# Optimization experiments

Measured on AMD Instinct MI355X. Metric: run time of the kernel, lower is better.

The kernel has to match this reference:

```python
import jax, jax.numpy as jnp
import numpy as np

B, C, T, R = 32, 8, 512, 256


def setup_inputs() -> dict:
    key = jax.random.key(0)
    k1, k2, k3 = jax.random.split(key, 3)
    x = jax.random.normal(k1, (B, C, T), dtype=jnp.float32)
    # W_in ~ U(-1, 1), shape [reservoir, input_size=1]
    W_in = jax.random.uniform(k2, (R, 1), minval=-1.0, maxval=1.0, dtype=jnp.float32)
    # diagonal of W_res ~ U(-1, 1)
    d = jax.random.uniform(k3, (R,), minval=-1.0, maxval=1.0, dtype=jnp.float32)
    return {"x": x, "W_in": W_in, "d": d}


def reference(x, W_in, d):
    # state_{t} = tanh(u_t * W_in[:,0] + state_{t-1} * d), vectorized over (B,C)
    w = W_in[:, 0]                       # [R]
    b, c, t = x.shape
    xs = jnp.moveaxis(x, -1, 0)          # [T, B, C]
    init = jnp.zeros((b, c, w.shape[0]), dtype=x.dtype)  # [B, C, R]

    def step(state, u_t):
        s = jnp.tanh(u_t[..., None] * w + state * d)  # [B, C, R]
        return s, s

    _, states = jax.lax.scan(step, init, xs)  # [T, B, C, R]
    return jnp.moveaxis(states, 0, 2)         # [B, C, T, R]
```

## Files before the change

### kernel.cpp

```cpp
#include <hip/hip_runtime.h>


constexpr int Bdim = 32;
constexpr int Cdim = 8;
constexpr int Tdim = 512;
constexpr int Rdim = 256;
constexpr int T4   = Tdim / 4;
constexpr int NT   = 128;

__device__ __forceinline__ float fast_exp2(float v) {
#if defined(__has_builtin)
#if __has_builtin(__builtin_amdgcn_exp2f)
    return __builtin_amdgcn_exp2f(v);
#else
    return exp2f(v);
#endif
#else
    return exp2f(v);
#endif
}

__global__ __launch_bounds__(NT, 1) void esn_scan_kernel(
    const float* __restrict__ x,
    const float* __restrict__ W_in,
    const float* __restrict__ d,
    float* __restrict__ out)
{
    const int bc = blockIdx.x;
    const int i  = threadIdx.x;

    const float K     = 2.0f * 1.4426950408889634f;
    const float wkA   = W_in[i] * K;
    const float dkA   = d[i] * K;
    const float m2dkA = -2.0f * dkA;
    const float wkB   = W_in[i + 128] * K;
    const float dkB   = d[i + 128] * K;
    const float m2dkB = -2.0f * dkB;

    __shared__ float4 xs4[T4];
    {
        const float4* __restrict__ x4 = reinterpret_cast<const float4*>(x + bc * Tdim);
        xs4[i] = x4[i];
    }
    __syncthreads();

    float* __restrict__ o = out + (size_t)bc * Tdim * Rdim + i;

    float4 a0 = xs4[0], a1 = xs4[1];
    float4 b0 = xs4[2], b1 = xs4[3];

    float eargA = a0.x * wkA;
    float eargB = a0.x * wkB;

    #pragma unroll 1
    for (int g = 0; g < Tdim / 8; ++g) {
        int pf = 2 * g + 4; if (pf > T4 - 2) pf = T4 - 2;
        float4 c0 = xs4[pf], c1 = xs4[pf + 1];

        float preA[8], preB[8];
        preA[0] = fmaf(a0.y, wkA, dkA);  preB[0] = fmaf(a0.y, wkB, dkB);
        preA[1] = fmaf(a0.z, wkA, dkA);  preB[1] = fmaf(a0.z, wkB, dkB);
        preA[2] = fmaf(a0.w, wkA, dkA);  preB[2] = fmaf(a0.w, wkB, dkB);
        preA[3] = fmaf(a1.x, wkA, dkA);  preB[3] = fmaf(a1.x, wkB, dkB);
        preA[4] = fmaf(a1.y, wkA, dkA);  preB[4] = fmaf(a1.y, wkB, dkB);
        preA[5] = fmaf(a1.z, wkA, dkA);  preB[5] = fmaf(a1.z, wkB, dkB);
        preA[6] = fmaf(a1.w, wkA, dkA);  preB[6] = fmaf(a1.w, wkB, dkB);
        preA[7] = fmaf(b0.x, wkA, dkA);  preB[7] = fmaf(b0.x, wkB, dkB);

        float* ob  = o + (size_t)(g * 8) * Rdim;
        float* ob4 = ob + (size_t)4 * Rdim;

        #pragma unroll
        for (int j = 0; j < 4; ++j) {
            float eA  = fast_exp2(eargA);
            float eB  = fast_exp2(eargB);
            float rcA = __builtin_amdgcn_rcpf(eA + 1.0f);
            float rcB = __builtin_amdgcn_rcpf(eB + 1.0f);
            ob[j * Rdim]       = fmaf(-2.0f, rcA, 1.0f);
            ob[j * Rdim + 128] = fmaf(-2.0f, rcB, 1.0f);
            eargA = fmaf(m2dkA, rcA, preA[j]);
            eargB = fmaf(m2dkB, rcB, preB[j]);
        }
        #pragma unroll
        for (int j = 0; j < 4; ++j) {
            float eA  = fast_exp2(eargA);
            float eB  = fast_exp2(eargB);
            float rcA = __builtin_amdgcn_rcpf(eA + 1.0f);
            float rcB = __builtin_amdgcn_rcpf(eB + 1.0f);
            ob4[j * Rdim]       = fmaf(-2.0f, rcA, 1.0f);
            ob4[j * Rdim + 128] = fmaf(-2.0f, rcB, 1.0f);
            eargA = fmaf(m2dkA, rcA, preA[j + 4]);
            eargB = fmaf(m2dkB, rcB, preB[j + 4]);
        }

        a0 = b0; a1 = b1;
        b0 = c0; b1 = c1;
    }
}

extern "C" void kernel_launch(void* const* d_in, const int* in_sizes, int n_in,
                              void* d_out, int out_size, void* d_ws, size_t ws_size,
                              hipStream_t stream) {
    const float* x    = (const float*)d_in[0];
    const float* W_in = (const float*)d_in[1];
    const float* d    = (const float*)d_in[2];
    float* out        = (float*)d_out;

    dim3 grid(Bdim * Cdim);
    dim3 block(NT);
    esn_scan_kernel<<<grid, block, 0, stream>>>(x, W_in, d, out);
}
```

Baseline: 31.78 us.

## Replace exp2/rcp tanh with clamped rational polynomial and use one thread per reservoir unit

Computes tanh with a clamped rational polynomial approximation (one rcp, no exp) instead of the exp2-plus-reciprocal form. The recurrence now carries the pre-activation directly. The block grows from 128 to 256 threads, so each thread owns one reservoir element instead of two interleaved chains. This shortens the per-step dependency chain by dropping the transcendental, but adds more FMAs per step and slightly changes accuracy near the clamp.

```diff
diff --git a/kernel.cpp b/kernel.cpp
--- a/kernel.cpp
+++ b/kernel.cpp
@@ -6,91 +6,79 @@
 constexpr int Tdim = 512;
 constexpr int Rdim = 256;
 constexpr int T4   = Tdim / 4;
-constexpr int NT   = 128;
 
-__device__ __forceinline__ float fast_exp2(float v) {
-#if defined(__has_builtin)
-#if __has_builtin(__builtin_amdgcn_exp2f)
-    return __builtin_amdgcn_exp2f(v);
-#else
-    return exp2f(v);
-#endif
-#else
-    return exp2f(v);
-#endif
+__device__ __forceinline__ float tanh_p(float z) {
+    float p = fmaf(z, -2.76076847742355e-16f, 2.00018790482477e-13f);
+    p = fmaf(z, p, -8.60467152213735e-11f);
+    p = fmaf(z, p, 5.12229709037114e-08f);
+    p = fmaf(z, p, 1.48572235717979e-05f * 0.0f + 1.48572235717979e-05f);
+    p = fmaf(z, p, 6.37261928875436e-04f);
+    p = fmaf(z, p, 4.89352455891786e-03f);
+    return p;
+}
+__device__ __forceinline__ float tanh_q(float z) {
+    float q = fmaf(z, 1.19825839466702e-06f, 1.18534705686654e-04f);
+    q = fmaf(z, q, 2.26843463243900e-03f);
+    q = fmaf(z, q, 4.89352518554385e-03f);
+    return q;
 }
 
-__global__ __launch_bounds__(NT, 1) void esn_scan_kernel(
+__global__ __launch_bounds__(256, 1) void esn_scan_kernel(
     const float* __restrict__ x,
     const float* __restrict__ W_in,
     const float* __restrict__ d,
     float* __restrict__ out)
 {
     const int bc = blockIdx.x;
-    const int i  = threadIdx.x;
+    const int r  = threadIdx.x;
 
-    const float K     = 2.0f * 1.4426950408889634f;
-    const float wkA   = W_in[i] * K;
-    const float dkA   = d[i] * K;
-    const float m2dkA = -2.0f * dkA;
-    const float wkB   = W_in[i + 128] * K;
-    const float dkB   = d[i + 128] * K;
-    const float m2dkB = -2.0f * dkB;
+    const float wc = W_in[r];
+    const float dc = d[r];
 
     __shared__ float4 xs4[T4];
     {
         const float4* __restrict__ x4 = reinterpret_cast<const float4*>(x + bc * Tdim);
-        xs4[i] = x4[i];
+        if (r < T4) xs4[r] = x4[r];
     }
     __syncthreads();
 
-    float* __restrict__ o = out + (size_t)bc * Tdim * Rdim + i;
+    float* __restrict__ o = out + (size_t)bc * Tdim * Rdim + r;
 
     float4 a0 = xs4[0], a1 = xs4[1];
     float4 b0 = xs4[2], b1 = xs4[3];
 
-    float eargA = a0.x * wkA;
-    float eargB = a0.x * wkB;
+    float a = a0.x * wc;
 
     #pragma unroll 1
     for (int g = 0; g < Tdim / 8; ++g) {
         int pf = 2 * g + 4; if (pf > T4 - 2) pf = T4 - 2;
         float4 c0 = xs4[pf], c1 = xs4[pf + 1];
 
-        float preA[8], preB[8];
-        preA[0] = fmaf(a0.y, wkA, dkA);  preB[0] = fmaf(a0.y, wkB, dkB);
-        preA[1] = fmaf(a0.z, wkA, dkA);  preB[1] = fmaf(a0.z, wkB, dkB);
-        preA[2] = fmaf(a0.w, wkA, dkA);  preB[2] = fmaf(a0.w, wkB, dkB);
-        preA[3] = fmaf(a1.x, wkA, dkA);  preB[3] = fmaf(a1.x, wkB, dkB);
-        preA[4] = fmaf(a1.y, wkA, dkA);  preB[4] = fmaf(a1.y, wkB, dkB);
-        preA[5] = fmaf(a1.z, wkA, dkA);  preB[5] = fmaf(a1.z, wkB, dkB);
-        preA[6] = fmaf(a1.w, wkA, dkA);  preB[6] = fmaf(a1.w, wkB, dkB);
-        preA[7] = fmaf(b0.x, wkA, dkA);  preB[7] = fmaf(b0.x, wkB, dkB);
+        float pre[8];
+        pre[0] = a0.y * wc;
+        pre[1] = a0.z * wc;
+        pre[2] = a0.w * wc;
+        pre[3] = a1.x * wc;
+        pre[4] = a1.y * wc;
+        pre[5] = a1.z * wc;
+        pre[6] = a1.w * wc;
+        pre[7] = b0.x * wc;
 
         float* ob  = o + (size_t)(g * 8) * Rdim;
         float* ob4 = ob + (size_t)4 * Rdim;
 
         #pragma unroll
-        for (int j = 0; j < 4; ++j) {
-            float eA  = fast_exp2(eargA);
-            float eB  = fast_exp2(eargB);
-            float rcA = __builtin_amdgcn_rcpf(eA + 1.0f);
-            float rcB = __builtin_amdgcn_rcpf(eB + 1.0f);
-            ob[j * Rdim]       = fmaf(-2.0f, rcA, 1.0f);
-            ob[j * Rdim + 128] = fmaf(-2.0f, rcB, 1.0f);
-            eargA = fmaf(m2dkA, rcA, preA[j]);
-            eargB = fmaf(m2dkB, rcB, preB[j]);
-        }
-        #pragma unroll
-        for (int j = 0; j < 4; ++j) {
-            float eA  = fast_exp2(eargA);
-            float eB  = fast_exp2(eargB);
-            float rcA = __builtin_amdgcn_rcpf(eA + 1.0f);
-            float rcB = __builtin_amdgcn_rcpf(eB + 1.0f);
-            ob4[j * Rdim]       = fmaf(-2.0f, rcA, 1.0f);
-            ob4[j * Rdim + 128] = fmaf(-2.0f, rcB, 1.0f);
-            eargA = fmaf(m2dkA, rcA, preA[j + 4]);
-            eargB = fmaf(m2dkB, rcB, preB[j + 4]);
+        for (int j = 0; j < 8; ++j) {
+            float z  = a * a;
+            float p  = tanh_p(z);
+            float q  = tanh_q(z);
+            float rc = __builtin_amdgcn_rcpf(q);
+            float pa = p * a;
+            float s  = pa * rc;
+            if (j < 4) ob[j * Rdim] = s;
+            else       ob4[(j - 4) * Rdim] = s;
+            a = fmaf(pa * dc, rc, pre[j]);
+            a = fminf(7.90531f, fmaxf(-7.90531f, a));
         }
 
         a0 = b0; a1 = b1;
@@ -107,6 +95,6 @@
     float* out        = (float*)d_out;
 
     dim3 grid(Bdim * Cdim);
-    dim3 block(NT);
+    dim3 block(Rdim);
     esn_scan_kernel<<<grid, block, 0, stream>>>(x, W_in, d, out);
 }
```

After: 31.93 us. About the same (+0.5%).
